# Kernel tuning notes

Hardware: AMD Instinct MI355X
Metric: run time of the kernel (lower is better)

The kernel has to match this reference:

```python
import jax, jax.numpy as jnp
import numpy as np

N, DEG, F_IN, H = 50000, 16, 128, 32
E = N * DEG


def _linear_params(key, out_f, in_f):
    kw, kb = jax.random.split(key)
    s = 1.0 / np.sqrt(in_f)
    W = jax.random.uniform(kw, (out_f, in_f), jnp.float32, -s, s)
    b = jax.random.uniform(kb, (out_f,), jnp.float32, -s, s)
    return W, b


def setup_inputs() -> dict:
    key = jax.random.key(0)
    ks = jax.random.split(key, 12)
    X = jax.random.normal(ks[0], (N, F_IN), jnp.float32)
    # DEG distinct nonzero offsets shared by all rows -> unique (src,dst) pairs,
    # so the COO tensor is already coalesced (no duplicate indices).
    offsets = jax.random.permutation(ks[1], jnp.arange(1, N))[:DEG]
    src = jnp.repeat(jnp.arange(N, dtype=jnp.int32), DEG)
    dst = ((src.reshape(N, DEG) + offsets[None, :].astype(jnp.int32)) % N).reshape(-1)
    D = jax.ops.segment_sum(jnp.ones((E,), jnp.float32), src, num_segments=N)
    wn1p, bn1p = _linear_params(ks[2], H, F_IN)      # convN1.pass_map
    wn1s, bn1s = _linear_params(ks[3], H, F_IN)      # convN1.self_map
    we1p, be1p = _linear_params(ks[4], H, 2 * H)     # convE1.pass_map
    we1s, be1s = _linear_params(ks[5], H, F_IN)      # convE1.self_map
    wn2p, bn2p = _linear_params(ks[6], H, H)         # convN2.pass_map
    wn2s, bn2s = _linear_params(ks[7], H, H)         # convN2.self_map
    we2p, be2p = _linear_params(ks[8], H, 2 * H)     # convE2.pass_map
    we2s, be2s = _linear_params(ks[9], H, H)         # convE2.self_map
    wc, bc = _linear_params(ks[10], 1, H)            # classifier
    return dict(X=X, src=src, dst=dst, D=D,
                wn1p=wn1p, bn1p=bn1p, wn1s=wn1s, bn1s=bn1s,
                we1p=we1p, be1p=be1p, we1s=we1s, be1s=be1s,
                wn2p=wn2p, bn2p=bn2p, wn2s=wn2s, bn2s=bn2s,
                we2p=we2p, be2p=be2p, we2s=we2s, be2s=be2s,
                wc=wc, bc=bc)


def reference(X, src, dst, D,
              wn1p, bn1p, wn1s, bn1s,
              we1p, be1p, we1s, be1s,
              wn2p, bn2p, wn2s, bn2s,
              we2p, be2p, we2s, be2s,
              wc, bc):
    n = X.shape[0]

    def node_conv(vals, Xn, wp, bp, ws, bs):
        # torch.sparse.sum(A, dim=1): sum edge values per source row
        Asum = jax.ops.segment_sum(vals, src, num_segments=n)
        return jax.nn.relu((Asum / D[:, None]) @ wp.T + bp + Xn @ ws.T + bs)

    def edge_conv(vals, Xn, wp, bp, ws, bs):
        X1, X2 = Xn[src], Xn[dst]
        Ef = jnp.concatenate([(X1 - X2) * 0.5, (X1 + X2) * 0.5], axis=-1)
        return jax.nn.relu(Ef @ wp.T + bp + vals @ ws.T + bs)

    # add_graph: edge features = |X[src] - X[dst]|
    vals0 = jnp.abs(X[src] - X[dst])            # (E, F_IN)
    X0 = jnp.zeros_like(X)                       # forward zeros node features
    Xn1 = node_conv(vals0, X0, wn1p, bn1p, wn1s, bn1s)   # (N, 32)
    vals1 = edge_conv(vals0, Xn1, we1p, be1p, we1s, be1s)  # (E, 32)
    Xn2 = node_conv(vals1, Xn1, wn2p, bn2p, wn2s, bn2s)  # (N, 32)
    vals2 = edge_conv(vals1, Xn2, we2p, be2p, we2s, be2s)  # (E, 32)
    SX = jax.nn.sigmoid(vals2 @ wc.T + bc)[:, 0]          # (E,)
    return SX
```

## Files before the change

### kernel.cpp

```cpp
#include <hip/hip_runtime.h>

#define DEG 16
#define F_IN 128
#define H 32

typedef __attribute__((ext_vector_type(8))) _Float16 f16x8;
typedef __attribute__((ext_vector_type(4))) float f32x4;
typedef __attribute__((ext_vector_type(4))) int i32x4;

union HS { _Float16 f; unsigned short s; };

__device__ __forceinline__ float relu_f(float x) { return fmaxf(x, 0.0f); }

__device__ __forceinline__ f16x8 habs8(f16x8 a) {
    union { f16x8 h; i32x4 i; } u; u.h = a;
#pragma unroll
    for (int k = 0; k < 4; ++k) u.i[k] &= 0x7FFF7FFF;
    return u.h;
}

__global__ __launch_bounds__(256) void k_xhalf(
    const float* __restrict__ X, _Float16* __restrict__ Xh, long n8)
{
    const long t = (long)blockIdx.x * 256 + threadIdx.x;
    if (t >= n8) return;
    const float4* p = (const float4*)X + t * 2;
    const float4 a = p[0], b = p[1];
    f16x8 h;
    h[0] = (_Float16)a.x; h[1] = (_Float16)a.y; h[2] = (_Float16)a.z; h[3] = (_Float16)a.w;
    h[4] = (_Float16)b.x; h[5] = (_Float16)b.y; h[6] = (_Float16)b.z; h[7] = (_Float16)b.w;
    *(f16x8*)(Xh + t * 8) = h;
}

__global__ __launch_bounds__(256) void k_prep(
    const float* __restrict__ we1s, const float* __restrict__ we1p,
    const float* __restrict__ be1p, const float* __restrict__ be1s,
    const float* __restrict__ we2p, const float* __restrict__ we2s,
    const float* __restrict__ be2p, const float* __restrict__ be2s,
    const float* __restrict__ wn1p, const float* __restrict__ bn1p,
    const float* __restrict__ bn1s,
    const float* __restrict__ wn2p, const float* __restrict__ bn2p,
    const float* __restrict__ wn2s, const float* __restrict__ bn2s,
    _Float16* __restrict__ Wcat1, _Float16* __restrict__ Wcat2,
    _Float16* __restrict__ Wn1ph,
    _Float16* __restrict__ Wn2ph, _Float16* __restrict__ Wn2sh,
    float* __restrict__ bias1, float* __restrict__ bias2,
    float* __restrict__ biasn1, float* __restrict__ biasn2)
{
    const int t0 = blockIdx.x * 256 + threadIdx.x;
    const int stride = gridDim.x * 256;
    for (int idx = t0; idx < 32 * 192; idx += stride) {
        const int n = idx / 192, k = idx - n * 192;
        float w;
        if (k < 128)       w = we1s[n * 128 + k];
        else if (k < 160)  w = 0.5f * we1p[n * 64 + (k - 128)];
        else               w = 0.5f * we1p[n * 64 + 32 + (k - 160)];
        Wcat1[idx] = (_Float16)w;
    }
    for (int idx = t0; idx < 32 * 96; idx += stride) {
        const int n = idx / 96, k = idx - n * 96;
        float w;
        if (k < 32)       w = 0.5f * we2p[n * 64 + k];
        else if (k < 64)  w = 0.5f * we2p[n * 64 + 32 + (k - 32)];
        else              w = we2s[n * 32 + (k - 64)];
        Wcat2[idx] = (_Float16)w;
    }
    for (int idx = t0; idx < 32 * 128; idx += stride)
        Wn1ph[idx] = (_Float16)wn1p[idx];
    for (int idx = t0; idx < 32 * 32; idx += stride) {
        Wn2ph[idx] = (_Float16)wn2p[idx];
        Wn2sh[idx] = (_Float16)wn2s[idx];
    }
    if (t0 < H) {
        bias1[t0]  = be1p[t0] + be1s[t0];
        bias2[t0]  = be2p[t0] + be2s[t0];
        biasn1[t0] = bn1p[t0] + bn1s[t0];
        biasn2[t0] = bn2p[t0] + bn2s[t0];
    }
}

__global__ __launch_bounds__(64, 4) void k_p1(
    const _Float16* __restrict__ Xh, const int* __restrict__ dst,
    const float* __restrict__ D,
    const _Float16* __restrict__ Wn1ph, const float* __restrict__ biasn1,
    _Float16* __restrict__ Xn1h, int N)
{
    const int lane = threadIdx.x;
    const int m = lane & 15, g = lane >> 4;
    const int i0 = blockIdx.x * 16;
    const int srow = (i0 + m < N) ? (i0 + m) : (N - 1);

    i32x4 dj4[4];
    {
        const i32x4* dp = (const i32x4*)(dst + (size_t)srow * DEG);
#pragma unroll
        for (int q = 0; q < 4; ++q) dj4[q] = dp[q];
    }
    f16x8 sv[4];
#pragma unroll
    for (int kb = 0; kb < 4; ++kb)
        sv[kb] = *(const f16x8*)(Xh + (size_t)srow * F_IN + kb * 32 + g * 8);
    f16x8 Bn[4][2];
#pragma unroll
    for (int kb = 0; kb < 4; ++kb)
#pragma unroll
        for (int t = 0; t < 2; ++t)
            Bn[kb][t] = *(const f16x8*)(Wn1ph + (t * 16 + m) * 128 + kb * 32 + g * 8);

    f16x8 tvc[4], tvn[4];
#pragma unroll
    for (int kb = 0; kb < 4; ++kb)
        tvc[kb] = *(const f16x8*)(Xh + (size_t)dj4[0][0] * F_IN + kb * 32 + g * 8);

    f32x4 cn0 = {0.f,0.f,0.f,0.f}, cn1 = {0.f,0.f,0.f,0.f};
#pragma unroll
    for (int j = 0; j < 16; ++j) {
        if (j < 15) {
            const int dn = dj4[(j + 1) >> 2][(j + 1) & 3];
#pragma unroll
            for (int kb = 0; kb < 4; ++kb)
                tvn[kb] = *(const f16x8*)(Xh + (size_t)dn * F_IN + kb * 32 + g * 8);
        }
#pragma unroll
        for (int kb = 0; kb < 4; ++kb) {
            const f16x8 a = habs8(sv[kb] - tvc[kb]);
            cn0 = __builtin_amdgcn_mfma_f32_16x16x32_f16(a, Bn[kb][0], cn0, 0, 0, 0);
            cn1 = __builtin_amdgcn_mfma_f32_16x16x32_f16(a, Bn[kb][1], cn1, 0, 0, 0);
        }
#pragma unroll
        for (int kb = 0; kb < 4; ++kb) tvc[kb] = tvn[kb];
    }
    const float bn0 = biasn1[m], bn1v = biasn1[16 + m];
#pragma unroll
    for (int r = 0; r < 4; ++r) {
        const int node = i0 + g * 4 + r;
        if (node < N) {
            const float invD = 1.0f / D[node];
            Xn1h[(size_t)node * H + m]      = (_Float16)relu_f(cn0[r] * invD + bn0);
            Xn1h[(size_t)node * H + 16 + m] = (_Float16)relu_f(cn1[r] * invD + bn1v);
        }
    }
}

__global__ __launch_bounds__(64, 3) void k_p2(
    const _Float16* __restrict__ Xh, const int* __restrict__ dst,
    const _Float16* __restrict__ Xn1h,
    const _Float16* __restrict__ Wcat1, const float* __restrict__ bias1,
    const _Float16* __restrict__ Wn2ph, const _Float16* __restrict__ Wn2sh,
    const float* __restrict__ biasn2, const float* __restrict__ D,
    _Float16* __restrict__ vals1, _Float16* __restrict__ Xn2h, int N)
{
    __shared__ unsigned short RP[16 * 40];
    const int lane = threadIdx.x;
    const int m = lane & 15, g = lane >> 4;
    const int i0 = blockIdx.x * 16;
    const int srow = (i0 + m < N) ? (i0 + m) : (N - 1);

    i32x4 dj4[4];
    {
        const i32x4* dp = (const i32x4*)(dst + (size_t)srow * DEG);
#pragma unroll
        for (int q = 0; q < 4; ++q) dj4[q] = dp[q];
    }
    const f16x8 x1 = *(const f16x8*)(Xn1h + (size_t)srow * H + g * 8);
    f16x8 sv[4];
#pragma unroll
    for (int kb = 0; kb < 4; ++kb)
        sv[kb] = *(const f16x8*)(Xh + (size_t)srow * F_IN + kb * 32 + g * 8);
    f16x8 Bf[6][2];
#pragma unroll
    for (int kb = 0; kb < 6; ++kb)
#pragma unroll
        for (int t = 0; t < 2; ++t)
            Bf[kb][t] = *(const f16x8*)(Wcat1 + (t * 16 + m) * 192 + kb * 32 + g * 8);

    f16x8 tvc[4], tvn[4], x2c, x2n;
    {
        const int d0 = dj4[0][0];
#pragma unroll
        for (int kb = 0; kb < 4; ++kb)
            tvc[kb] = *(const f16x8*)(Xh + (size_t)d0 * F_IN + kb * 32 + g * 8);
        x2c = *(const f16x8*)(Xn1h + (size_t)d0 * H + g * 8);
    }

    const float b0 = bias1[m], b1v = bias1[16 + m];
    f32x4 sB0 = {0.f,0.f,0.f,0.f}, sB1 = {0.f,0.f,0.f,0.f};
    const int rr = lane >> 2, qq = lane & 3;
#pragma unroll
    for (int j = 0; j < 16; ++j) {
        if (j < 15) {
            const int dn = dj4[(j + 1) >> 2][(j + 1) & 3];
#pragma unroll
            for (int kb = 0; kb < 4; ++kb)
                tvn[kb] = *(const f16x8*)(Xh + (size_t)dn * F_IN + kb * 32 + g * 8);
            x2n = *(const f16x8*)(Xn1h + (size_t)dn * H + g * 8);
        }
        f32x4 c0 = {0.f,0.f,0.f,0.f}, c1 = {0.f,0.f,0.f,0.f};
#pragma unroll
        for (int kb = 0; kb < 4; ++kb) {
            const f16x8 a = habs8(sv[kb] - tvc[kb]);
            c0 = __builtin_amdgcn_mfma_f32_16x16x32_f16(a, Bf[kb][0], c0, 0, 0, 0);
            c1 = __builtin_amdgcn_mfma_f32_16x16x32_f16(a, Bf[kb][1], c1, 0, 0, 0);
        }
        const f16x8 ad = x1 - x2c;
        const f16x8 aS = x1 + x2c;
        c0 = __builtin_amdgcn_mfma_f32_16x16x32_f16(ad, Bf[4][0], c0, 0, 0, 0);
        c1 = __builtin_amdgcn_mfma_f32_16x16x32_f16(ad, Bf[4][1], c1, 0, 0, 0);
        c0 = __builtin_amdgcn_mfma_f32_16x16x32_f16(aS, Bf[5][0], c0, 0, 0, 0);
        c1 = __builtin_amdgcn_mfma_f32_16x16x32_f16(aS, Bf[5][1], c1, 0, 0, 0);
#pragma unroll
        for (int r = 0; r < 4; ++r) {
            const float v0 = relu_f(c0[r] + b0);
            const float v1 = relu_f(c1[r] + b1v);
            HS h0, h1; h0.f = (_Float16)v0; h1.f = (_Float16)v1;
            RP[(g * 4 + r) * 40 + m]      = h0.s;
            RP[(g * 4 + r) * 40 + 16 + m] = h1.s;
            sB0[r] += v0; sB1[r] += v1;
        }
        const size_t tb = ((size_t)blockIdx.x * 16 + j) * 512;
        const i32x4 v = *(const i32x4*)(RP + rr * 40 + qq * 8);
        *(i32x4*)(vals1 + tb + rr * 32 + qq * 8) = v;
#pragma unroll
        for (int kb = 0; kb < 4; ++kb) tvc[kb] = tvn[kb];
        x2c = x2n;
    }
    _Float16* RPh = (_Float16*)RP;
#pragma unroll
    for (int r = 0; r < 4; ++r) {
        const int node = i0 + g * 4 + r;
        const float invD = 1.0f / D[(node < N) ? node : (N - 1)];
        RPh[(g * 4 + r) * 40 + m]      = (_Float16)(sB0[r] * invD);
        RPh[(g * 4 + r) * 40 + 16 + m] = (_Float16)(sB1[r] * invD);
    }
    const f16x8 aF = *(const f16x8*)(RPh + m * 40 + g * 8);
    f16x8 Bp[2], Bs2[2];
#pragma unroll
    for (int t = 0; t < 2; ++t) {
        Bp[t]  = *(const f16x8*)(Wn2ph + (t * 16 + m) * H + g * 8);
        Bs2[t] = *(const f16x8*)(Wn2sh + (t * 16 + m) * H + g * 8);
    }
    f32x4 c0 = {0.f,0.f,0.f,0.f}, c1 = {0.f,0.f,0.f,0.f};
    c0 = __builtin_amdgcn_mfma_f32_16x16x32_f16(aF, Bp[0], c0, 0, 0, 0);
    c1 = __builtin_amdgcn_mfma_f32_16x16x32_f16(aF, Bp[1], c1, 0, 0, 0);
    c0 = __builtin_amdgcn_mfma_f32_16x16x32_f16(x1, Bs2[0], c0, 0, 0, 0);
    c1 = __builtin_amdgcn_mfma_f32_16x16x32_f16(x1, Bs2[1], c1, 0, 0, 0);
    const float bp0 = biasn2[m], bp1 = biasn2[16 + m];
#pragma unroll
    for (int r = 0; r < 4; ++r) {
        const int node = i0 + g * 4 + r;
        if (node < N) {
            Xn2h[(size_t)node * H + m]      = (_Float16)relu_f(c0[r] + bp0);
            Xn2h[(size_t)node * H + 16 + m] = (_Float16)relu_f(c1[r] + bp1);
        }
    }
}

__global__ __launch_bounds__(64, 4) void k_p3(
    const _Float16* __restrict__ Xn2h, const int* __restrict__ dst,
    const _Float16* __restrict__ vals1,
    const _Float16* __restrict__ Wcat2, const float* __restrict__ bias2,
    const float* __restrict__ wc, const float* __restrict__ bc,
    float* __restrict__ out, int N)
{
    __shared__ float outS[16 * 16];
    const int lane = threadIdx.x;
    const int m = lane & 15, g = lane >> 4;
    const int i0 = blockIdx.x * 16;
    const int srow = (i0 + m < N) ? (i0 + m) : (N - 1);

    i32x4 dj4[4];
    {
        const i32x4* dp = (const i32x4*)(dst + (size_t)srow * DEG);
#pragma unroll
        for (int q = 0; q < 4; ++q) dj4[q] = dp[q];
    }
    const f16x8 x1 = *(const f16x8*)(Xn2h + (size_t)srow * H + g * 8);
    f16x8 Bf[3][2];
#pragma unroll
    for (int kb = 0; kb < 3; ++kb)
#pragma unroll
        for (int t = 0; t < 2; ++t)
            Bf[kb][t] = *(const f16x8*)(Wcat2 + (t * 16 + m) * 96 + kb * 32 + g * 8);

    f16x8 x2c, x2n, avc, avn;
    {
        const int d0 = dj4[0][0];
        x2c = *(const f16x8*)(Xn2h + (size_t)d0 * H + g * 8);
        avc = *(const f16x8*)(vals1 + ((size_t)blockIdx.x * 16 + 0) * 512 + m * 32 + g * 8);
    }
    const float b0 = bias2[m], b1v = bias2[16 + m];
    const float w0 = wc[m], w1 = wc[16 + m];
#pragma unroll
    for (int j = 0; j < 16; ++j) {
        if (j < 15) {
            const int dn = dj4[(j + 1) >> 2][(j + 1) & 3];
            x2n = *(const f16x8*)(Xn2h + (size_t)dn * H + g * 8);
            avn = *(const f16x8*)(vals1 + ((size_t)blockIdx.x * 16 + j + 1) * 512 + m * 32 + g * 8);
        }
        const f16x8 ad = x1 - x2c;
        const f16x8 aS = x1 + x2c;
        f32x4 c0 = {0.f,0.f,0.f,0.f}, c1 = {0.f,0.f,0.f,0.f};
        c0 = __builtin_amdgcn_mfma_f32_16x16x32_f16(ad,  Bf[0][0], c0, 0, 0, 0);
        c1 = __builtin_amdgcn_mfma_f32_16x16x32_f16(ad,  Bf[0][1], c1, 0, 0, 0);
        c0 = __builtin_amdgcn_mfma_f32_16x16x32_f16(aS,  Bf[1][0], c0, 0, 0, 0);
        c1 = __builtin_amdgcn_mfma_f32_16x16x32_f16(aS,  Bf[1][1], c1, 0, 0, 0);
        c0 = __builtin_amdgcn_mfma_f32_16x16x32_f16(avc, Bf[2][0], c0, 0, 0, 0);
        c1 = __builtin_amdgcn_mfma_f32_16x16x32_f16(avc, Bf[2][1], c1, 0, 0, 0);

        float sr[4];
#pragma unroll
        for (int r = 0; r < 4; ++r)
            sr[r] = relu_f(c0[r] + b0) * w0 + relu_f(c1[r] + b1v) * w1;
#pragma unroll
        for (int mask = 1; mask < 16; mask <<= 1) {
#pragma unroll
            for (int r = 0; r < 4; ++r)
                sr[r] += __shfl_xor(sr[r], mask);
        }
        if (m == 0) {
#pragma unroll
            for (int r = 0; r < 4; ++r)
                outS[(g * 4 + r) * 16 + j] = sr[r];
        }
        x2c = x2n; avc = avn;
    }
    {
        const float bcv = bc[0];
        const float* s = outS + lane * 4;
        float4 o;
        o.x = 1.0f / (1.0f + __expf(-(s[0] + bcv)));
        o.y = 1.0f / (1.0f + __expf(-(s[1] + bcv)));
        o.z = 1.0f / (1.0f + __expf(-(s[2] + bcv)));
        o.w = 1.0f / (1.0f + __expf(-(s[3] + bcv)));
        if (i0 + 16 <= N || (i0 + (lane >> 2)) < N)
            *(float4*)(out + (size_t)i0 * DEG + lane * 4) = o;
    }
}

extern "C" void kernel_launch(void* const* d_in, const int* in_sizes, int n_in,
                              void* d_out, int out_size, void* d_ws, size_t ws_size,
                              hipStream_t stream)
{
    const float* X    = (const float*)d_in[0];
    const int*   dst  = (const int*)  d_in[2];
    const float* D    = (const float*)d_in[3];
    const float* wn1p = (const float*)d_in[4];
    const float* bn1p = (const float*)d_in[5];
    const float* bn1s = (const float*)d_in[7];
    const float* we1p = (const float*)d_in[8];
    const float* be1p = (const float*)d_in[9];
    const float* we1s = (const float*)d_in[10];
    const float* be1s = (const float*)d_in[11];
    const float* wn2p = (const float*)d_in[12];
    const float* bn2p = (const float*)d_in[13];
    const float* wn2s = (const float*)d_in[14];
    const float* bn2s = (const float*)d_in[15];
    const float* we2p = (const float*)d_in[16];
    const float* be2p = (const float*)d_in[17];
    const float* we2s = (const float*)d_in[18];
    const float* be2s = (const float*)d_in[19];
    const float* wc   = (const float*)d_in[20];
    const float* bc   = (const float*)d_in[21];

    const int N = in_sizes[3];
    const int nbW = (N + 15) / 16;
    const size_t Epad = (size_t)nbW * 16 * DEG;

    char* w = (char*)d_ws;
    _Float16* vals1 = (_Float16*)w;  w += Epad * H * 2;
    _Float16* Xh    = (_Float16*)w;  w += (size_t)N * F_IN * 2;
    _Float16* Xn1h  = (_Float16*)w;  w += (size_t)N * H * 2;
    _Float16* Xn2h  = (_Float16*)w;  w += (size_t)N * H * 2;
    _Float16* Wcat1 = (_Float16*)w;  w += 32 * 192 * 2;
    _Float16* Wcat2 = (_Float16*)w;  w += 32 * 96 * 2;
    _Float16* Wn1ph = (_Float16*)w;  w += 32 * 128 * 2;
    _Float16* Wn2ph = (_Float16*)w;  w += 32 * 32 * 2;
    _Float16* Wn2sh = (_Float16*)w;  w += 32 * 32 * 2;
    float* bias1  = (float*)w;       w += H * 4;
    float* bias2  = (float*)w;       w += H * 4;
    float* biasn1 = (float*)w;       w += H * 4;
    float* biasn2 = (float*)w;       w += H * 4;
    float* outp = (float*)d_out;

    const long n8 = (long)N * F_IN / 8;
    const int nbX = (int)((n8 + 255) / 256);

    k_xhalf<<<nbX, 256, 0, stream>>>(X, Xh, n8);
    k_prep<<<32, 256, 0, stream>>>(we1s, we1p, be1p, be1s, we2p, we2s, be2p, be2s,
                                   wn1p, bn1p, bn1s, wn2p, bn2p, wn2s, bn2s,
                                   Wcat1, Wcat2, Wn1ph, Wn2ph, Wn2sh,
                                   bias1, bias2, biasn1, biasn2);
    k_p1<<<nbW, 64, 0, stream>>>(Xh, dst, D, Wn1ph, biasn1, Xn1h, N);
    k_p2<<<nbW, 64, 0, stream>>>(Xh, dst, Xn1h, Wcat1, bias1, Wn2ph, Wn2sh,
                                 biasn2, D, vals1, Xn2h, N);
    k_p3<<<nbW, 64, 0, stream>>>(Xn2h, dst, vals1, Wcat2, bias2, wc, bc, outp, N);
}
```

Baseline: 207.4 us.

## Compute edge self-map partial in p1 and stop re-gathering X in p2

k_p1 already gathers |X[src]-X[dst]| for every edge. It now also runs that operand through the convE1 self-map weights and stores the fp16 partial products to a buffer that is shared in place with vals1. k_p2 no longer re-gathers the 128-wide X rows. It loads the precomputed partial, adds the Xn1 pass-map MFMAs, and overwrites the buffer with vals1. k_p3 prefetches two steps ahead with a double buffer. The change trades a large second gather of X for extra register pressure in p1 and an extra fp16 write and read of the intermediate, which also rounds the partial to fp16.

```diff
diff --git a/kernel.cpp b/kernel.cpp
--- a/kernel.cpp
+++ b/kernel.cpp
@@ -8,7 +8,8 @@
 typedef __attribute__((ext_vector_type(4))) float f32x4;
 typedef __attribute__((ext_vector_type(4))) int i32x4;
 
-union HS { _Float16 f; unsigned short s; };
+union HS  { _Float16 f; unsigned short s; };
+union HF4 { _Float16 h[4]; uint2 u; };
 
 __device__ __forceinline__ float relu_f(float x) { return fmaxf(x, 0.0f); }
 
@@ -79,11 +80,12 @@
     }
 }
 
-__global__ __launch_bounds__(64, 4) void k_p1(
+__global__ __launch_bounds__(64, 3) void k_p1(
     const _Float16* __restrict__ Xh, const int* __restrict__ dst,
     const float* __restrict__ D,
-    const _Float16* __restrict__ Wn1ph, const float* __restrict__ biasn1,
-    _Float16* __restrict__ Xn1h, int N)
+    const _Float16* __restrict__ Wcat1, const _Float16* __restrict__ Wn1ph,
+    const float* __restrict__ biasn1,
+    _Float16* __restrict__ t1h, _Float16* __restrict__ Xn1h, int N)
 {
     const int lane = threadIdx.x;
     const int m = lane & 15, g = lane >> 4;
@@ -100,12 +102,14 @@
 #pragma unroll
     for (int kb = 0; kb < 4; ++kb)
         sv[kb] = *(const f16x8*)(Xh + (size_t)srow * F_IN + kb * 32 + g * 8);
-    f16x8 Bn[4][2];
+    f16x8 Bs[4][2], Bn[4][2];
 #pragma unroll
     for (int kb = 0; kb < 4; ++kb)
 #pragma unroll
-        for (int t = 0; t < 2; ++t)
+        for (int t = 0; t < 2; ++t) {
+            Bs[kb][t] = *(const f16x8*)(Wcat1 + (t * 16 + m) * 192 + kb * 32 + g * 8);
             Bn[kb][t] = *(const f16x8*)(Wn1ph + (t * 16 + m) * 128 + kb * 32 + g * 8);
+        }
 
     f16x8 tvc[4], tvn[4];
 #pragma unroll
@@ -121,12 +125,23 @@
             for (int kb = 0; kb < 4; ++kb)
                 tvn[kb] = *(const f16x8*)(Xh + (size_t)dn * F_IN + kb * 32 + g * 8);
         }
+        f32x4 cs0 = {0.f,0.f,0.f,0.f}, cs1 = {0.f,0.f,0.f,0.f};
 #pragma unroll
         for (int kb = 0; kb < 4; ++kb) {
             const f16x8 a = habs8(sv[kb] - tvc[kb]);
+            cs0 = __builtin_amdgcn_mfma_f32_16x16x32_f16(a, Bs[kb][0], cs0, 0, 0, 0);
+            cs1 = __builtin_amdgcn_mfma_f32_16x16x32_f16(a, Bs[kb][1], cs1, 0, 0, 0);
             cn0 = __builtin_amdgcn_mfma_f32_16x16x32_f16(a, Bn[kb][0], cn0, 0, 0, 0);
             cn1 = __builtin_amdgcn_mfma_f32_16x16x32_f16(a, Bn[kb][1], cn1, 0, 0, 0);
         }
+        const size_t tb = ((size_t)blockIdx.x * 16 + j) * 512;
+        HF4 a;
+#pragma unroll
+        for (int r = 0; r < 4; ++r) a.h[r] = (_Float16)cs0[r];
+        *(uint2*)(t1h + tb + lane * 4) = a.u;
+#pragma unroll
+        for (int r = 0; r < 4; ++r) a.h[r] = (_Float16)cs1[r];
+        *(uint2*)(t1h + tb + 256 + lane * 4) = a.u;
 #pragma unroll
         for (int kb = 0; kb < 4; ++kb) tvc[kb] = tvn[kb];
     }
@@ -142,13 +157,13 @@
     }
 }
 
-__global__ __launch_bounds__(64, 3) void k_p2(
-    const _Float16* __restrict__ Xh, const int* __restrict__ dst,
-    const _Float16* __restrict__ Xn1h,
+__global__ __launch_bounds__(64, 4) void k_p2(
+    const int* __restrict__ dst, const _Float16* __restrict__ Xn1h,
     const _Float16* __restrict__ Wcat1, const float* __restrict__ bias1,
     const _Float16* __restrict__ Wn2ph, const _Float16* __restrict__ Wn2sh,
     const float* __restrict__ biasn2, const float* __restrict__ D,
-    _Float16* __restrict__ vals1, _Float16* __restrict__ Xn2h, int N)
+    _Float16* t1v1,
+    _Float16* __restrict__ Xn2h, int N)
 {
     __shared__ unsigned short RP[16 * 40];
     const int lane = threadIdx.x;
@@ -163,26 +178,22 @@
         for (int q = 0; q < 4; ++q) dj4[q] = dp[q];
     }
     const f16x8 x1 = *(const f16x8*)(Xn1h + (size_t)srow * H + g * 8);
-    f16x8 sv[4];
-#pragma unroll
-    for (int kb = 0; kb < 4; ++kb)
-        sv[kb] = *(const f16x8*)(Xh + (size_t)srow * F_IN + kb * 32 + g * 8);
-    f16x8 Bf[6][2];
-#pragma unroll
-    for (int kb = 0; kb < 6; ++kb)
+    f16x8 Bf[2][2];
+#pragma unroll
+    for (int kb = 0; kb < 2; ++kb)
 #pragma unroll
         for (int t = 0; t < 2; ++t)
-            Bf[kb][t] = *(const f16x8*)(Wcat1 + (t * 16 + m) * 192 + kb * 32 + g * 8);
-
-    f16x8 tvc[4], tvn[4], x2c, x2n;
+            Bf[kb][t] = *(const f16x8*)(Wcat1 + (t * 16 + m) * 192 + (4 + kb) * 32 + g * 8);
+
+    f16x8 x2c, x2n;
+    uint2 u0c, u1c, u0n, u1n;
     {
         const int d0 = dj4[0][0];
-#pragma unroll
-        for (int kb = 0; kb < 4; ++kb)
-            tvc[kb] = *(const f16x8*)(Xh + (size_t)d0 * F_IN + kb * 32 + g * 8);
         x2c = *(const f16x8*)(Xn1h + (size_t)d0 * H + g * 8);
-    }
-
+        const size_t tb = ((size_t)blockIdx.x * 16) * 512;
+        u0c = *(const uint2*)(t1v1 + tb + lane * 4);
+        u1c = *(const uint2*)(t1v1 + tb + 256 + lane * 4);
+    }
     const float b0 = bias1[m], b1v = bias1[16 + m];
     f32x4 sB0 = {0.f,0.f,0.f,0.f}, sB1 = {0.f,0.f,0.f,0.f};
     const int rr = lane >> 2, qq = lane & 3;
@@ -190,24 +201,24 @@
     for (int j = 0; j < 16; ++j) {
         if (j < 15) {
             const int dn = dj4[(j + 1) >> 2][(j + 1) & 3];
-#pragma unroll
-            for (int kb = 0; kb < 4; ++kb)
-                tvn[kb] = *(const f16x8*)(Xh + (size_t)dn * F_IN + kb * 32 + g * 8);
             x2n = *(const f16x8*)(Xn1h + (size_t)dn * H + g * 8);
-        }
-        f32x4 c0 = {0.f,0.f,0.f,0.f}, c1 = {0.f,0.f,0.f,0.f};
-#pragma unroll
-        for (int kb = 0; kb < 4; ++kb) {
-            const f16x8 a = habs8(sv[kb] - tvc[kb]);
-            c0 = __builtin_amdgcn_mfma_f32_16x16x32_f16(a, Bf[kb][0], c0, 0, 0, 0);
-            c1 = __builtin_amdgcn_mfma_f32_16x16x32_f16(a, Bf[kb][1], c1, 0, 0, 0);
-        }
+            const size_t tbn = ((size_t)blockIdx.x * 16 + j + 1) * 512;
+            u0n = *(const uint2*)(t1v1 + tbn + lane * 4);
+            u1n = *(const uint2*)(t1v1 + tbn + 256 + lane * 4);
+        }
+        f32x4 c0, c1;
+        { HF4 a; a.u = u0c;
+#pragma unroll
+          for (int r = 0; r < 4; ++r) c0[r] = (float)a.h[r];
+          a.u = u1c;
+#pragma unroll
+          for (int r = 0; r < 4; ++r) c1[r] = (float)a.h[r]; }
         const f16x8 ad = x1 - x2c;
         const f16x8 aS = x1 + x2c;
-        c0 = __builtin_amdgcn_mfma_f32_16x16x32_f16(ad, Bf[4][0], c0, 0, 0, 0);
-        c1 = __builtin_amdgcn_mfma_f32_16x16x32_f16(ad, Bf[4][1], c1, 0, 0, 0);
-        c0 = __builtin_amdgcn_mfma_f32_16x16x32_f16(aS, Bf[5][0], c0, 0, 0, 0);
-        c1 = __builtin_amdgcn_mfma_f32_16x16x32_f16(aS, Bf[5][1], c1, 0, 0, 0);
+        c0 = __builtin_amdgcn_mfma_f32_16x16x32_f16(ad, Bf[0][0], c0, 0, 0, 0);
+        c1 = __builtin_amdgcn_mfma_f32_16x16x32_f16(ad, Bf[0][1], c1, 0, 0, 0);
+        c0 = __builtin_amdgcn_mfma_f32_16x16x32_f16(aS, Bf[1][0], c0, 0, 0, 0);
+        c1 = __builtin_amdgcn_mfma_f32_16x16x32_f16(aS, Bf[1][1], c1, 0, 0, 0);
 #pragma unroll
         for (int r = 0; r < 4; ++r) {
             const float v0 = relu_f(c0[r] + b0);
@@ -219,10 +230,8 @@
         }
         const size_t tb = ((size_t)blockIdx.x * 16 + j) * 512;
         const i32x4 v = *(const i32x4*)(RP + rr * 40 + qq * 8);
-        *(i32x4*)(vals1 + tb + rr * 32 + qq * 8) = v;
-#pragma unroll
-        for (int kb = 0; kb < 4; ++kb) tvc[kb] = tvn[kb];
-        x2c = x2n;
+        *(i32x4*)(t1v1 + tb + rr * 32 + qq * 8) = v;
+        x2c = x2n; u0c = u0n; u1c = u1n;
     }
     _Float16* RPh = (_Float16*)RP;
 #pragma unroll
@@ -282,30 +291,34 @@
         for (int t = 0; t < 2; ++t)
             Bf[kb][t] = *(const f16x8*)(Wcat2 + (t * 16 + m) * 96 + kb * 32 + g * 8);
 
-    f16x8 x2c, x2n, avc, avn;
-    {
-        const int d0 = dj4[0][0];
-        x2c = *(const f16x8*)(Xn2h + (size_t)d0 * H + g * 8);
-        avc = *(const f16x8*)(vals1 + ((size_t)blockIdx.x * 16 + 0) * 512 + m * 32 + g * 8);
+    f16x8 x2b[2], avb[2];
+#pragma unroll
+    for (int s = 0; s < 2; ++s) {
+        const int dn = dj4[s >> 2][s & 3];
+        x2b[s] = *(const f16x8*)(Xn2h + (size_t)dn * H + g * 8);
+        avb[s] = *(const f16x8*)(vals1 + ((size_t)blockIdx.x * 16 + s) * 512 + m * 32 + g * 8);
     }
     const float b0 = bias2[m], b1v = bias2[16 + m];
     const float w0 = wc[m], w1 = wc[16 + m];
 #pragma unroll
     for (int j = 0; j < 16; ++j) {
-        if (j < 15) {
-            const int dn = dj4[(j + 1) >> 2][(j + 1) & 3];
-            x2n = *(const f16x8*)(Xn2h + (size_t)dn * H + g * 8);
-            avn = *(const f16x8*)(vals1 + ((size_t)blockIdx.x * 16 + j + 1) * 512 + m * 32 + g * 8);
-        }
-        const f16x8 ad = x1 - x2c;
-        const f16x8 aS = x1 + x2c;
+        const int s = j & 1;
+        const f16x8 x2 = x2b[s];
+        const f16x8 av = avb[s];
+        if (j < 14) {
+            const int dn = dj4[(j + 2) >> 2][(j + 2) & 3];
+            x2b[s] = *(const f16x8*)(Xn2h + (size_t)dn * H + g * 8);
+            avb[s] = *(const f16x8*)(vals1 + ((size_t)blockIdx.x * 16 + j + 2) * 512 + m * 32 + g * 8);
+        }
+        const f16x8 ad = x1 - x2;
+        const f16x8 aS = x1 + x2;
         f32x4 c0 = {0.f,0.f,0.f,0.f}, c1 = {0.f,0.f,0.f,0.f};
-        c0 = __builtin_amdgcn_mfma_f32_16x16x32_f16(ad,  Bf[0][0], c0, 0, 0, 0);
-        c1 = __builtin_amdgcn_mfma_f32_16x16x32_f16(ad,  Bf[0][1], c1, 0, 0, 0);
-        c0 = __builtin_amdgcn_mfma_f32_16x16x32_f16(aS,  Bf[1][0], c0, 0, 0, 0);
-        c1 = __builtin_amdgcn_mfma_f32_16x16x32_f16(aS,  Bf[1][1], c1, 0, 0, 0);
-        c0 = __builtin_amdgcn_mfma_f32_16x16x32_f16(avc, Bf[2][0], c0, 0, 0, 0);
-        c1 = __builtin_amdgcn_mfma_f32_16x16x32_f16(avc, Bf[2][1], c1, 0, 0, 0);
+        c0 = __builtin_amdgcn_mfma_f32_16x16x32_f16(ad, Bf[0][0], c0, 0, 0, 0);
+        c1 = __builtin_amdgcn_mfma_f32_16x16x32_f16(ad, Bf[0][1], c1, 0, 0, 0);
+        c0 = __builtin_amdgcn_mfma_f32_16x16x32_f16(aS, Bf[1][0], c0, 0, 0, 0);
+        c1 = __builtin_amdgcn_mfma_f32_16x16x32_f16(aS, Bf[1][1], c1, 0, 0, 0);
+        c0 = __builtin_amdgcn_mfma_f32_16x16x32_f16(av, Bf[2][0], c0, 0, 0, 0);
+        c1 = __builtin_amdgcn_mfma_f32_16x16x32_f16(av, Bf[2][1], c1, 0, 0, 0);
 
         float sr[4];
 #pragma unroll
@@ -322,7 +335,6 @@
             for (int r = 0; r < 4; ++r)
                 outS[(g * 4 + r) * 16 + j] = sr[r];
         }
-        x2c = x2n; avc = avn;
     }
     {
         const float bcv = bc[0];
@@ -367,7 +379,7 @@
     const size_t Epad = (size_t)nbW * 16 * DEG;
 
     char* w = (char*)d_ws;
-    _Float16* vals1 = (_Float16*)w;  w += Epad * H * 2;
+    _Float16* t1v1  = (_Float16*)w;  w += Epad * H * 2;
     _Float16* Xh    = (_Float16*)w;  w += (size_t)N * F_IN * 2;
     _Float16* Xn1h  = (_Float16*)w;  w += (size_t)N * H * 2;
     _Float16* Xn2h  = (_Float16*)w;  w += (size_t)N * H * 2;
@@ -390,8 +402,8 @@
                                    wn1p, bn1p, bn1s, wn2p, bn2p, wn2s, bn2s,
                                    Wcat1, Wcat2, Wn1ph, Wn2ph, Wn2sh,
                                    bias1, bias2, biasn1, biasn2);
-    k_p1<<<nbW, 64, 0, stream>>>(Xh, dst, D, Wn1ph, biasn1, Xn1h, N);
-    k_p2<<<nbW, 64, 0, stream>>>(Xh, dst, Xn1h, Wcat1, bias1, Wn2ph, Wn2sh,
-                                 biasn2, D, vals1, Xn2h, N);
-    k_p3<<<nbW, 64, 0, stream>>>(Xn2h, dst, vals1, Wcat2, bias2, wc, bc, outp, N);
-}
+    k_p1<<<nbW, 64, 0, stream>>>(Xh, dst, D, Wcat1, Wn1ph, biasn1, t1v1, Xn1h, N);
+    k_p2<<<nbW, 64, 0, stream>>>(dst, Xn1h, Wcat1, bias1, Wn2ph, Wn2sh,
+                                 biasn2, D, t1v1, Xn2h, N);
+    k_p3<<<nbW, 64, 0, stream>>>(Xn2h, dst, t1v1, Wcat2, bias2, wc, bc, outp, N);
+}
```

Result: faster. 199.7 us (-3.7%).
